# Performance work log

Hardware: AMD Instinct MI355X
Metric: run time of the kernel (lower is better)

The kernel has to match this reference:

```python
import jax, jax.numpy as jnp
import numpy as np

L, H, E, FFN, V, BLOCK = 8, 16, 1024, 4096, 32000, 2048
D = E // H  # head dim = 64
EPS = 1e-5
STD = 0.02

def _ln(x, g, b):
    m = jnp.mean(x, axis=-1, keepdims=True)
    v = jnp.var(x, axis=-1, keepdims=True)
    return (x - m) * jax.lax.rsqrt(v + EPS) * g + b

def setup_inputs() -> dict:
    key = jax.random.key(0)
    ks = jax.random.split(key, 12)
    n = lambda k, shape: (jax.random.normal(k, shape, dtype=jnp.float32) * STD)
    return {
        "idx": jax.random.randint(ks[0], (2, 2048), 0, V),
        "tok_emb": n(ks[1], (V, E)),
        "pos_emb": n(ks[2], (BLOCK, E)),
        # attention weights stored [in, out] so we use x @ W
        "wq": n(ks[3], (L, E, E)),
        "wk": n(ks[4], (L, E, E)),
        "wv": n(ks[5], (L, E, E)),
        "wo": n(ks[6], (L, E, E)),
        "bo": jnp.zeros((L, E), jnp.float32),
        "w1": n(ks[7], (L, E, FFN)),
        "b1": jnp.zeros((L, FFN), jnp.float32),
        "w2": n(ks[8], (L, FFN, E)),
        "b2": jnp.zeros((L, E), jnp.float32),
        "ln1_g": jnp.ones((L, E), jnp.float32),
        "ln1_b": jnp.zeros((L, E), jnp.float32),
        "ln2_g": jnp.ones((L, E), jnp.float32),
        "ln2_b": jnp.zeros((L, E), jnp.float32),
        "lnf_g": jnp.ones((E,), jnp.float32),
        "lnf_b": jnp.zeros((E,), jnp.float32),
    }

def reference(idx, tok_emb, pos_emb, wq, wk, wv, wo, bo, w1, b1, w2, b2,
              ln1_g, ln1_b, ln2_g, ln2_b, lnf_g, lnf_b):
    B, T = idx.shape
    x = tok_emb[idx] + pos_emb[:T]  # [B,T,E]
    causal = jnp.tril(jnp.ones((T, T), dtype=bool))
    scale = 1.0 / np.sqrt(D)

    def step(x, p):
        (wq_, wk_, wv_, wo_, bo_, w1_, b1_, w2_, b2_,
         g1, be1, g2, be2) = p
        h = _ln(x, g1, be1)
        q = (h @ wq_).reshape(B, T, H, D)
        k = (h @ wk_).reshape(B, T, H, D)
        v = (h @ wv_).reshape(B, T, H, D)
        scores = jnp.einsum('bthd,bshd->bhts', q, k) * scale  # [B,H,T,T]
        scores = jnp.where(causal, scores, -jnp.inf)
        w = jax.nn.softmax(scores, axis=-1)
        attn = jnp.einsum('bhts,bshd->bthd', w, v).reshape(B, T, E)
        x = x + attn @ wo_ + bo_
        h2 = _ln(x, g2, be2)
        x = x + jax.nn.relu(h2 @ w1_ + b1_) @ w2_ + b2_
        return x, None

    x, _ = jax.lax.scan(step, x, (wq, wk, wv, wo, bo, w1, b1, w2, b2,
                                  ln1_g, ln1_b, ln2_g, ln2_b))
    x = _ln(x, lnf_g, lnf_b)
    logits = x @ tok_emb.T  # tied weights
    return logits
```

## Files before the change

kernel.cpp:

```cpp
#include <hip/hip_runtime.h>
#include <hip/hip_bf16.h>
#include <cstdint>
#include <cstddef>

#define LAYERS   8
#define HEADS    16
#define EMB      1024
#define FFND     4096
#define VOCAB    32000
#define SEQ      2048
#define NBATCH   2
#define MROWS    (NBATCH*SEQ)
#define HDIM     64
#define QKVSTR   3072
#define LN_EPS   1e-5f

typedef __hip_bfloat16 bf16;
typedef short short8 __attribute__((ext_vector_type(8)));
typedef float f32x4  __attribute__((ext_vector_type(4)));

__device__ __forceinline__ void async_copy16(const bf16* g, bf16* l) {
  __builtin_amdgcn_global_load_lds(
      (const __attribute__((address_space(1))) void*)g,
      (__attribute__((address_space(3))) void*)l, 16, 0, 0);
}

__device__ __forceinline__ uint32_t bfbits(float x) {
  __hip_bfloat16 h = __float2bfloat16(x);
  return (uint32_t)reinterpret_cast<uint16_t&>(h);
}

struct __align__(8) B4 { bf16 a, b, c, d; };

__global__ void k_f32_to_bf16(const float* __restrict__ in, bf16* __restrict__ out, long n4) {
  long i = (long)blockIdx.x * blockDim.x + threadIdx.x;
  const long stride = (long)gridDim.x * blockDim.x;
  for (; i < n4; i += stride) {
    float4 v = reinterpret_cast<const float4*>(in)[i];
    B4 o;
    o.a = __float2bfloat16(v.x);
    o.b = __float2bfloat16(v.y);
    o.c = __float2bfloat16(v.z);
    o.d = __float2bfloat16(v.w);
    reinterpret_cast<B4*>(out)[i] = o;
  }
}

__global__ void k_embed(const int* __restrict__ idx, const float* __restrict__ tok,
                        const float* __restrict__ pos, float* __restrict__ x) {
  const int row  = blockIdx.x;
  const int tpos = row & (SEQ - 1);
  const int token = idx[row];
  const float4* te = (const float4*)(tok + (long)token * EMB);
  const float4* pe = (const float4*)(pos + (long)tpos * EMB);
  float4* xo = (float4*)(x + (long)row * EMB);
  for (int i = threadIdx.x; i < EMB / 4; i += blockDim.x) {
    float4 a = te[i], b = pe[i];
    a.x += b.x; a.y += b.y; a.z += b.z; a.w += b.w;
    xo[i] = a;
  }
}

__global__ void k_transpose_w(const float* __restrict__ in, bf16* __restrict__ out,
                              int K, int N) {
  __shared__ float tile[32][33];
  const int n0 = blockIdx.x * 32, k0 = blockIdx.y * 32;
  const int tx = threadIdx.x, ty = threadIdx.y;
  for (int i = 0; i < 32; i += 8)
    tile[ty + i][tx] = in[(long)(k0 + ty + i) * N + n0 + tx];
  __syncthreads();
  for (int i = 0; i < 32; i += 8)
    out[(long)(n0 + ty + i) * K + k0 + tx] = __float2bfloat16(tile[tx][ty + i]);
}

__global__ void k_transpose_w4(const float* __restrict__ wq, const float* __restrict__ wk,
                               const float* __restrict__ wv, const float* __restrict__ wo,
                               bf16* __restrict__ qkvT, bf16* __restrict__ woT) {
  __shared__ float tile[32][33];
  const float* in;
  bf16* out;
  switch (blockIdx.z) {
    case 0:  in = wq; out = qkvT;               break;
    case 1:  in = wk; out = qkvT + EMB * EMB;   break;
    case 2:  in = wv; out = qkvT + 2 * EMB * EMB; break;
    default: in = wo; out = woT;                break;
  }
  const int n0 = blockIdx.x * 32, k0 = blockIdx.y * 32;
  const int tx = threadIdx.x, ty = threadIdx.y;
  for (int i = 0; i < 32; i += 8)
    tile[ty + i][tx] = in[(long)(k0 + ty + i) * EMB + n0 + tx];
  __syncthreads();
  for (int i = 0; i < 32; i += 8)
    out[(long)(n0 + ty + i) * EMB + k0 + tx] = __float2bfloat16(tile[tx][ty + i]);
}

__global__ void k_transpose_v(const bf16* __restrict__ v, int vstr, bf16* __restrict__ vt) {
  __shared__ bf16 tile[32][33];
  const int bh = blockIdx.z;
  const int b = bh >> 4, h = bh & 15;
  const int t0 = blockIdx.x * 32, d0 = blockIdx.y * 32;
  const int tx = threadIdx.x, ty = threadIdx.y;
  for (int i = 0; i < 32; i += 8)
    tile[ty + i][tx] = v[(long)(b * SEQ + t0 + ty + i) * vstr + h * HDIM + d0 + tx];
  __syncthreads();
  for (int i = 0; i < 32; i += 8)
    vt[(long)(bh * HDIM + d0 + ty + i) * SEQ + t0 + tx] = tile[tx][ty + i];
}

__global__ __launch_bounds__(256)
void k_layernorm(const float* __restrict__ x, const float* __restrict__ g,
                 const float* __restrict__ b, bf16* __restrict__ out) {
  const long row = blockIdx.x;
  const float* xr = x + row * EMB;
  const int t = threadIdx.x;
  float xv[4];
  float s = 0.f, sq = 0.f;
#pragma unroll
  for (int i = 0; i < 4; i++) {
    xv[i] = xr[t + i * 256];
    s += xv[i];
    sq += xv[i] * xv[i];
  }
#pragma unroll
  for (int m = 1; m < 64; m <<= 1) { s += __shfl_xor(s, m); sq += __shfl_xor(sq, m); }
  __shared__ float rs_[4], rq_[4];
  const int wid = t >> 6;
  if ((t & 63) == 0) { rs_[wid] = s; rq_[wid] = sq; }
  __syncthreads();
  s  = rs_[0] + rs_[1] + rs_[2] + rs_[3];
  sq = rq_[0] + rq_[1] + rq_[2] + rq_[3];
  const float mean = s * (1.f / EMB);
  const float var  = sq * (1.f / EMB) - mean * mean;
  const float rstd = rsqrtf(var + LN_EPS);
#pragma unroll
  for (int i = 0; i < 4; i++) {
    const int c = t + i * 256;
    out[row * EMB + c] = __float2bfloat16((xv[i] - mean) * rstd * g[c] + b[c]);
  }
}

template<int MODE>
__global__ __launch_bounds__(512, 2)
void gemm256(const bf16* __restrict__ A, const bf16* __restrict__ Bt,
             int M, int N, int K,
             bf16* __restrict__ outB, float* __restrict__ outF,
             const float* __restrict__ bias) {
  extern __shared__ __align__(16) char smem[];
  char* const smA = smem;
  char* const smB = smem + 65536;

  const int t    = threadIdx.x;
  const int lane = t & 63;
  const int wid  = t >> 6;
  const int wr   = wid >> 2;
  const int wc   = wid & 3;
  const int lrow = lane & 15;
  const int ks16 = (lane >> 4) * 16;
  const int rswz = (lrow & 7) << 4;

  int lin = blockIdx.x * gridDim.y + blockIdx.y;
  { const int nwg = gridDim.x * gridDim.y; const int per = nwg >> 3;
    lin = (lin & 7) * per + (lin >> 3); }
  const int gx8  = gridDim.x * 8;
  const int half = lin / gx8;
  const int rem  = lin - half * gx8;
  const long bm  = (long)(half * 8 + (rem & 7)) * 256;
  const long bn  = (long)(rem >> 3) * 256;
  const int NT = K >> 6;

  const int row0 = wid * 8 + (lane >> 3);
  const int col0 = ((lane & 7) ^ (lane >> 3)) * 8;
  const int row1 = row0 + 64;
  const int dst0 = wid * 1024;
  const int dst1 = 8192 + wid * 1024;
  const bf16* const gA = A  + bm * K;
  const bf16* const gB = Bt + bn * K;

  auto STG = [&](char* ring, const bf16* g_, int tile, int h) {
    char* slot = ring + (((tile << 1) + h) & 3) * 16384;
    const bf16* sb = g_ + ((long)h * 128) * K + (long)tile * 64;
    async_copy16(sb + (long)row0 * K + col0, (bf16*)(slot + dst0));
    async_copy16(sb + (long)row1 * K + col0, (bf16*)(slot + dst1));
  };
  auto LDA8 = [&](int u, int m, int kk) -> short8 {
    const int off = (m * 16 + lrow) * 128 + ((kk * 64 + ks16) ^ rswz);
    return *reinterpret_cast<const short8*>(smA + (((u << 1) + wr) & 3) * 16384 + off);
  };
  auto LDB8 = [&](int u, int n, int kk) -> short8 {
    const int off = ((wc & 1) * 64 + n * 16 + lrow) * 128 + ((kk * 64 + ks16) ^ rswz);
    return *reinterpret_cast<const short8*>(smB + (((u << 1) + (wc >> 1)) & 3) * 16384 + off);
  };
#define MF(a_, b_, c_) __builtin_amdgcn_mfma_f32_16x16x32_bf16(a_, b_, c_, 0, 0, 0)

  f32x4 acc[8][4] = {};

  STG(smB, gB, 0, 0); STG(smB, gB, 0, 1);
  STG(smA, gA, 0, 0); STG(smA, gA, 0, 1);
  STG(smB, gB, 1, 0); STG(smB, gB, 1, 1);
  asm volatile("s_waitcnt vmcnt(4)" ::: "memory");
  __builtin_amdgcn_s_barrier();

  short8 bq[4][2];
  for (int u = 0; u < NT; u++) {
#pragma unroll
    for (int n = 0; n < 4; n++) { bq[n][0] = LDB8(u, n, 0); bq[n][1] = LDB8(u, n, 1); }
    short8 a0 = LDA8(u, 0, 0), a1 = LDA8(u, 0, 1), a2 = LDA8(u, 1, 0), a3 = LDA8(u, 1, 1);
    if (u + 1 < NT) STG(smA, gA, u + 1, 0);
    __builtin_amdgcn_s_barrier();
    asm volatile("s_waitcnt lgkmcnt(0)" ::: "memory");
    __builtin_amdgcn_sched_barrier(0);
    __builtin_amdgcn_s_setprio(1);
#pragma unroll
    for (int n = 0; n < 4; n++) {
      acc[0][n] = MF(a0, bq[n][0], acc[0][n]); acc[0][n] = MF(a1, bq[n][1], acc[0][n]);
      acc[1][n] = MF(a2, bq[n][0], acc[1][n]); acc[1][n] = MF(a3, bq[n][1], acc[1][n]);
    }
    __builtin_amdgcn_s_setprio(0);
    __builtin_amdgcn_s_barrier();

    a0 = LDA8(u, 2, 0); a1 = LDA8(u, 2, 1); a2 = LDA8(u, 3, 0); a3 = LDA8(u, 3, 1);
    if (u + 1 < NT) STG(smA, gA, u + 1, 1);
    __builtin_amdgcn_s_barrier();
    asm volatile("s_waitcnt lgkmcnt(0)" ::: "memory");
    __builtin_amdgcn_sched_barrier(0);
    __builtin_amdgcn_s_setprio(1);
#pragma unroll
    for (int n = 0; n < 4; n++) {
      acc[2][n] = MF(a0, bq[n][0], acc[2][n]); acc[2][n] = MF(a1, bq[n][1], acc[2][n]);
      acc[3][n] = MF(a2, bq[n][0], acc[3][n]); acc[3][n] = MF(a3, bq[n][1], acc[3][n]);
    }
    __builtin_amdgcn_s_setprio(0);
    __builtin_amdgcn_s_barrier();

    a0 = LDA8(u, 4, 0); a1 = LDA8(u, 4, 1); a2 = LDA8(u, 5, 0); a3 = LDA8(u, 5, 1);
    if (u + 2 < NT) STG(smB, gB, u + 2, 0);
    __builtin_amdgcn_s_barrier();
    asm volatile("s_waitcnt lgkmcnt(0)" ::: "memory");
    __builtin_amdgcn_sched_barrier(0);
    __builtin_amdgcn_s_setprio(1);
#pragma unroll
    for (int n = 0; n < 4; n++) {
      acc[4][n] = MF(a0, bq[n][0], acc[4][n]); acc[4][n] = MF(a1, bq[n][1], acc[4][n]);
      acc[5][n] = MF(a2, bq[n][0], acc[5][n]); acc[5][n] = MF(a3, bq[n][1], acc[5][n]);
    }
    __builtin_amdgcn_s_setprio(0);
    __builtin_amdgcn_s_barrier();

    a0 = LDA8(u, 6, 0); a1 = LDA8(u, 6, 1); a2 = LDA8(u, 7, 0); a3 = LDA8(u, 7, 1);
    if (u + 2 < NT) STG(smB, gB, u + 2, 1);
    __builtin_amdgcn_s_barrier();
    asm volatile("s_waitcnt lgkmcnt(0)" ::: "memory");
    __builtin_amdgcn_sched_barrier(0);
    __builtin_amdgcn_s_setprio(1);
#pragma unroll
    for (int n = 0; n < 4; n++) {
      acc[6][n] = MF(a0, bq[n][0], acc[6][n]); acc[6][n] = MF(a1, bq[n][1], acc[6][n]);
      acc[7][n] = MF(a2, bq[n][0], acc[7][n]); acc[7][n] = MF(a3, bq[n][1], acc[7][n]);
    }
    __builtin_amdgcn_s_setprio(0);
    if (u + 2 < NT) { asm volatile("s_waitcnt vmcnt(4)" ::: "memory"); }
    else            { asm volatile("s_waitcnt vmcnt(0)" ::: "memory"); }
    __builtin_amdgcn_s_barrier();
  }

  const long rb = bm + wr * 128 + (lane >> 4) * 4;
  const long cb = bn + wc * 64 + lrow;
#pragma unroll
  for (int m = 0; m < 8; m++) {
#pragma unroll
    for (int n = 0; n < 4; n++) {
      const long col = cb + n * 16;
#pragma unroll
      for (int r = 0; r < 4; r++) {
        const long row = rb + m * 16 + r;
        float v = acc[m][n][r];
        if (MODE == 0) {
          outB[row * N + col] = __float2bfloat16(v);
        } else if (MODE == 2) {
          v += bias[col];
          outB[row * N + col] = __float2bfloat16(v > 0.f ? v : 0.f);
        } else {
          outF[row * N + col] = v;
        }
      }
    }
  }
#undef MF
}

#define BM 128
#define BN 128
#define BK 32

__global__ __launch_bounds__(256)
void gemm_bt(const bf16* __restrict__ A, const bf16* __restrict__ Bt,
             int M, int N, int K,
             float* __restrict__ outF, const float* __restrict__ bias) {
  __shared__ __align__(16) bf16 lA[2][BM * BK];
  __shared__ __align__(16) bf16 lB[2][BN * BK];
  const int t    = threadIdx.x;
  const int lane = t & 63;
  const int wid  = t >> 6;
  const int wr   = wid >> 1;
  const int wc   = wid & 1;
  const long bm  = (long)blockIdx.y * BM;
  const long bn  = (long)blockIdx.x * BN;

  f32x4 acc[4][4] = {};

  const long arow = t >> 2;
  const int  acol = (((t & 3) ^ ((t >> 2) & 3)) * 8);
  const bf16* gA = A  + (bm + arow) * K + acol;
  const bf16* gB = Bt + (bn + arow) * K + acol;
  const long astep = 64L * K;

  auto STGBT = [&](int buf, int k0) {
    async_copy16(gA + k0,         &lA[buf][wid * 512]);
    async_copy16(gA + k0 + astep, &lA[buf][wid * 512 + 2048]);
    async_copy16(gB + k0,         &lB[buf][wid * 512]);
    async_copy16(gB + k0 + astep, &lB[buf][wid * 512 + 2048]);
  };

  STGBT(0, 0);
  __syncthreads();

  int cur = 0;
  for (int k0 = 0; k0 < K; k0 += BK) {
    if (k0 + BK < K) STGBT(cur ^ 1, k0 + BK);

    const int ksel = (((lane >> 4) ^ (lane & 3)) * 8);
    short8 af[4], bfv[4];
#pragma unroll
    for (int i = 0; i < 4; i++) {
      af[i]  = *reinterpret_cast<const short8*>(&lA[cur][(wr * 64 + i * 16 + (lane & 15)) * BK + ksel]);
      bfv[i] = *reinterpret_cast<const short8*>(&lB[cur][(wc * 64 + i * 16 + (lane & 15)) * BK + ksel]);
    }
#pragma unroll
    for (int i = 0; i < 4; i++)
#pragma unroll
      for (int j = 0; j < 4; j++)
        acc[i][j] = __builtin_amdgcn_mfma_f32_16x16x32_bf16(af[i], bfv[j], acc[i][j], 0, 0, 0);
    __syncthreads();
    cur ^= 1;
  }

  const long rbase = bm + wr * 64 + (lane >> 4) * 4;
  const long cbase = bn + wc * 64 + (lane & 15);
#pragma unroll
  for (int i = 0; i < 4; i++) {
#pragma unroll
    for (int j = 0; j < 4; j++) {
      const long col = cbase + j * 16;
#pragma unroll
      for (int r = 0; r < 4; r++) {
        const long row = rbase + i * 16 + r;
        outF[row * N + col] += acc[i][j][r] + bias[col];
      }
    }
  }
}

__global__ __launch_bounds__(256)
void k_attn(const bf16* __restrict__ qkv, const bf16* __restrict__ vt, bf16* __restrict__ o) {
  const int qt = gridDim.x - 1 - blockIdx.x;
  const int bh = blockIdx.y;
  const int b  = bh >> 4;
  const int h  = bh & 15;
  const int t0b = qt * 128;
  const int tid = threadIdx.x;
  const int w    = tid >> 6;
  const int lane = tid & 63;
  const int lg = lane >> 4;
  const int li = lane & 15;
  const int t0w = t0b + w * 32;

  __shared__ __align__(16) bf16 Kl[2][64 * 64];
  __shared__ __align__(16) bf16 Vl[2][64 * 64];
  __shared__ __align__(16) bf16 Pl[4][32 * 64];

  const bf16* qbase = qkv + (long)(b * SEQ) * QKVSTR + h * HDIM;
  const bf16* kbase = qkv + (long)(b * SEQ) * QKVSTR + EMB + h * HDIM;
  const bf16* vbase = vt + (long)bh * HDIM * SEQ;

  short8 qf[2][2];
#pragma unroll
  for (int f = 0; f < 2; f++) {
    const bf16* qrow = qbase + (long)(t0w + f * 16 + li) * QKVSTR;
    qf[f][0] = *reinterpret_cast<const short8*>(&qrow[lg * 8]);
    qf[f][1] = *reinterpret_cast<const short8*>(&qrow[32 + lg * 8]);
  }

  f32x4 oacc[2][4] = {};
  float mrow[2] = {-1e30f, -1e30f}, lrow[2] = {0.f, 0.f};

  const int nkt = (t0b >> 6) + 1;
  const int l8  = lane >> 3;
  const int sl8 = ((lane & 7) ^ l8) * 8;

  char* const Pw = (char*)&Pl[w][0];
  const int pswz = (li & 7) << 4;

#pragma unroll
  for (int sh = 0; sh < 2; sh++) {
    const int r = sh * 32 + w * 8 + l8;
    async_copy16(kbase + (long)r * QKVSTR + sl8, &Kl[0][(sh * 32 + w * 8) * 64]);
    async_copy16(vbase + (long)r * SEQ + sl8,    &Vl[0][(sh * 32 + w * 8) * 64]);
  }
  __syncthreads();

  int cur = 0;
  for (int kt = 0; kt <= nkt; kt++) {
    const int s0 = kt * 64;
    if (kt < nkt) {
      const int s0n = s0 + 64;
      bf16* Kn = &Kl[cur ^ 1][0];
      bf16* Vn = &Vl[cur ^ 1][0];
#pragma unroll
      for (int sh = 0; sh < 2; sh++) {
        const int r = sh * 32 + w * 8 + l8;
        async_copy16(kbase + (long)(s0n + r) * QKVSTR + sl8, Kn + (sh * 32 + w * 8) * 64);
        async_copy16(vbase + (long)r * SEQ + s0n + sl8,      Vn + (sh * 32 + w * 8) * 64);
      }
    }

    f32x4 s[2][4] = {};
#pragma unroll
    for (int kk = 0; kk < 2; kk++)
#pragma unroll
      for (int sf = 0; sf < 4; sf++) {
        const short8 kf = *reinterpret_cast<const short8*>(
            &Kl[cur][(sf * 16 + li) * 64 + ((((kk << 2) | lg) ^ (li & 7)) * 8)]);
        s[0][sf] = __builtin_amdgcn_mfma_f32_16x16x32_bf16(kf, qf[0][kk], s[0][sf], 0, 0, 0);
        s[1][sf] = __builtin_amdgcn_mfma_f32_16x16x32_bf16(kf, qf[1][kk], s[1][sf], 0, 0, 0);
      }

    const bool diag = (kt >= nkt - 1);
#pragma unroll
    for (int f = 0; f < 2; f++)
#pragma unroll
      for (int sf = 0; sf < 4; sf++)
#pragma unroll
        for (int r = 0; r < 4; r++) {
          float val = s[f][sf][r] * 0.18033688011112042f;
          if (diag && (s0 + sf * 16 + lg * 4 + r > t0w + f * 16 + li)) val = -1e30f;
          s[f][sf][r] = val;
        }

#pragma unroll
    for (int f = 0; f < 2; f++) {
      float mx = -1e30f;
#pragma unroll
      for (int sf = 0; sf < 4; sf++)
        mx = fmaxf(mx, fmaxf(fmaxf(s[f][sf][0], s[f][sf][1]), fmaxf(s[f][sf][2], s[f][sf][3])));
      mx = fmaxf(mx, __shfl_xor(mx, 16));
      mx = fmaxf(mx, __shfl_xor(mx, 32));
      const float mnew = fmaxf(mrow[f], mx);
      const float alpha = exp2f(mrow[f] - mnew);
      mrow[f] = mnew;
      float rs = 0.f;
#pragma unroll
      for (int sf = 0; sf < 4; sf++)
#pragma unroll
        for (int r = 0; r < 4; r++) {
          const float pv = exp2f(s[f][sf][r] - mnew);
          s[f][sf][r] = pv;
          rs += pv;
        }
      rs += __shfl_xor(rs, 16);
      rs += __shfl_xor(rs, 32);
      lrow[f] = lrow[f] * alpha + rs;
#pragma unroll
      for (int d = 0; d < 4; d++)
#pragma unroll
        for (int r = 0; r < 4; r++) oacc[f][d][r] *= alpha;

#pragma unroll
      for (int sf = 0; sf < 4; sf++) {
        uint2 pw2;
        pw2.x = (bfbits(s[f][sf][1]) << 16) | bfbits(s[f][sf][0]);
        pw2.y = (bfbits(s[f][sf][3]) << 16) | bfbits(s[f][sf][2]);
        *reinterpret_cast<uint2*>(Pw + (f * 16 + li) * 128 + ((sf * 32 + lg * 8) ^ pswz)) = pw2;
      }
    }

#pragma unroll
    for (int kk = 0; kk < 2; kk++) {
      const short8 pb0 = *reinterpret_cast<const short8*>(
          Pw + li * 128 + ((kk * 64 + lg * 16) ^ pswz));
      const short8 pb1 = *reinterpret_cast<const short8*>(
          Pw + (16 + li) * 128 + ((kk * 64 + lg * 16) ^ pswz));
#pragma unroll
      for (int d = 0; d < 4; d++) {
        const short8 vf = *reinterpret_cast<const short8*>(
            &Vl[cur][(d * 16 + li) * 64 + ((((kk << 2) | lg) ^ (li & 7)) * 8)]);
        oacc[0][d] = __builtin_amdgcn_mfma_f32_16x16x32_bf16(vf, pb0, oacc[0][d], 0, 0, 0);
        oacc[1][d] = __builtin_amdgcn_mfma_f32_16x16x32_bf16(vf, pb1, oacc[1][d], 0, 0, 0);
      }
    }

    __syncthreads();
    cur ^= 1;
  }

#pragma unroll
  for (int f = 0; f < 2; f++) {
    const float inv = 1.f / lrow[f];
    bf16* orow = o + (long)(b * SEQ + t0w + f * 16 + li) * EMB + h * HDIM;
#pragma unroll
    for (int d = 0; d < 4; d++) {
      uint2 ow;
      ow.x = (bfbits(oacc[f][d][1] * inv) << 16) | bfbits(oacc[f][d][0] * inv);
      ow.y = (bfbits(oacc[f][d][3] * inv) << 16) | bfbits(oacc[f][d][2] * inv);
      *reinterpret_cast<uint2*>(&orow[d * 16 + lg * 4]) = ow;
    }
  }
}

extern "C" void kernel_launch(void* const* d_in, const int* in_sizes, int n_in,
                              void* d_out, int out_size, void* d_ws, size_t ws_size,
                              hipStream_t stream) {
  (void)in_sizes; (void)n_in; (void)out_size; (void)ws_size;
  const int*   idx = (const int*)  d_in[0];
  const float* tok = (const float*)d_in[1];
  const float* pos = (const float*)d_in[2];
  const float* wq  = (const float*)d_in[3];
  const float* wk  = (const float*)d_in[4];
  const float* wv  = (const float*)d_in[5];
  const float* wo  = (const float*)d_in[6];
  const float* bo  = (const float*)d_in[7];
  const float* w1  = (const float*)d_in[8];
  const float* b1  = (const float*)d_in[9];
  const float* w2  = (const float*)d_in[10];
  const float* b2  = (const float*)d_in[11];
  const float* g1  = (const float*)d_in[12];
  const float* be1 = (const float*)d_in[13];
  const float* g2  = (const float*)d_in[14];
  const float* be2 = (const float*)d_in[15];
  const float* gf  = (const float*)d_in[16];
  const float* bef = (const float*)d_in[17];
  float* out = (float*)d_out;

  (void)hipFuncSetAttribute((const void*)gemm256<0>, hipFuncAttributeMaxDynamicSharedMemorySize, 131072);
  (void)hipFuncSetAttribute((const void*)gemm256<2>, hipFuncAttributeMaxDynamicSharedMemorySize, 131072);
  (void)hipFuncSetAttribute((const void*)gemm256<3>, hipFuncAttributeMaxDynamicSharedMemorySize, 131072);

  char* p = (char*)d_ws;
  auto take = [&p](size_t bytes) { char* r = p; p += (bytes + 255) & ~(size_t)255; return r; };
  float* xf   = (float*)take((size_t)MROWS * EMB * 4);
  bf16*  hb   = (bf16*) take((size_t)MROWS * EMB * 2);
  bf16*  qkvb = (bf16*) take((size_t)MROWS * QKVSTR * 2);
  bf16*  vtb  = (bf16*) take((size_t)MROWS * EMB * 2);
  bf16*  ab   = (bf16*) take((size_t)MROWS * EMB * 2);
  bf16*  fb   = (bf16*) take((size_t)MROWS * FFND * 2);
  bf16*  wqkvT= (bf16*) take((size_t)QKVSTR * EMB * 2);
  bf16*  woT  = (bf16*) take((size_t)EMB * EMB * 2);
  bf16*  w1T  = (bf16*) take((size_t)FFND * EMB * 2);
  bf16*  w2T  = (bf16*) take((size_t)EMB * FFND * 2);
  bf16*  tokT = (bf16*) take((size_t)VOCAB * EMB * 2);

  k_f32_to_bf16<<<2048, 256, 0, stream>>>(tok, tokT, (long)VOCAB * EMB / 4);
  k_embed<<<MROWS, 256, 0, stream>>>(idx, tok, pos, xf);

  const dim3 tb(32, 8);

  for (int l = 0; l < LAYERS; l++) {
    const size_t we = (size_t)l * EMB * EMB;
    const size_t wfo = (size_t)l * EMB * FFND;
    k_transpose_w4<<<dim3(EMB / 32, EMB / 32, 4), tb, 0, stream>>>(
        wq + we, wk + we, wv + we, wo + we, wqkvT, woT);
    k_transpose_w<<<dim3(FFND / 32, EMB / 32),  tb, 0, stream>>>(w1 + wfo, w1T, EMB,  FFND);
    k_transpose_w<<<dim3(EMB / 32,  FFND / 32), tb, 0, stream>>>(w2 + wfo, w2T, FFND, EMB);

    k_layernorm<<<MROWS, 256, 0, stream>>>(xf, g1 + l * EMB, be1 + l * EMB, hb);
    gemm256<0><<<dim3(QKVSTR / 256, MROWS / 256), 512, 131072, stream>>>(
        hb, wqkvT, MROWS, QKVSTR, EMB, qkvb, nullptr, nullptr);
    k_transpose_v<<<dim3(SEQ / 32, HDIM / 32, NBATCH * HEADS), tb, 0, stream>>>(qkvb + 2 * EMB, QKVSTR, vtb);
    k_attn<<<dim3(SEQ / 128, NBATCH * HEADS), 256, 0, stream>>>(qkvb, vtb, ab);
    gemm_bt<<<dim3(EMB / BN, MROWS / BM), 256, 0, stream>>>(ab, woT, MROWS, EMB, EMB, xf, bo + l * EMB);
    k_layernorm<<<MROWS, 256, 0, stream>>>(xf, g2 + l * EMB, be2 + l * EMB, hb);
    gemm256<2><<<dim3(FFND / 256, MROWS / 256), 512, 131072, stream>>>(
        hb, w1T, MROWS, FFND, EMB, fb, nullptr, b1 + l * FFND);
    gemm_bt<<<dim3(EMB / BN, MROWS / BM), 256, 0, stream>>>(fb, w2T, MROWS, EMB, FFND, xf, b2 + l * EMB);
  }

  k_layernorm<<<MROWS, 256, 0, stream>>>(xf, gf, bef, hb);
  gemm256<3><<<dim3(VOCAB / 256, MROWS / 256), 512, 131072, stream>>>(
      hb, tokT, MROWS, VOCAB, EMB, nullptr, out, nullptr);
}
```

Baseline: 3.020 ms.

## Split-K residual GEMMs with atomics, fold Q scale, lazy softmax rescaling

The Wo and W2 residual GEMMs are split over K into two z-slices that accumulate into the fp32 residual with atomic adds. This doubles the grid from 256 blocks so more compute units stay busy. The softmax scale is folded into the Q projection epilogue, so attention only masks diagonal tiles. The online-softmax rescale now runs only when some row max grows by more than 8, which skips most alpha multiplies at the cost of atomic traffic and bounded numeric drift.

New measurement: 2.713 ms. -10.2%, faster.

```diff
diff --git a/kernel.cpp b/kernel.cpp
--- a/kernel.cpp
+++ b/kernel.cpp
@@ -14,6 +14,7 @@
 #define HDIM     64
 #define QKVSTR   3072
 #define LN_EPS   1e-5f
+#define QSCALE   0.18033688011112042f
 
 typedef __hip_bfloat16 bf16;
 typedef short short8 __attribute__((ext_vector_type(8)));
@@ -275,6 +276,7 @@
         const long row = rb + m * 16 + r;
         float v = acc[m][n][r];
         if (MODE == 0) {
+          if (col < EMB) v *= QSCALE;
           outB[row * N + col] = __float2bfloat16(v);
         } else if (MODE == 2) {
           v += bias[col];
@@ -305,13 +307,15 @@
   const int wc   = wid & 1;
   const long bm  = (long)blockIdx.y * BM;
   const long bn  = (long)blockIdx.x * BN;
+  const int  kz  = blockIdx.z;
+  const int  Kh  = K >> 1;
 
   f32x4 acc[4][4] = {};
 
   const long arow = t >> 2;
   const int  acol = (((t & 3) ^ ((t >> 2) & 3)) * 8);
-  const bf16* gA = A  + (bm + arow) * K + acol;
-  const bf16* gB = Bt + (bn + arow) * K + acol;
+  const bf16* gA = A  + (bm + arow) * K + kz * Kh + acol;
+  const bf16* gB = Bt + (bn + arow) * K + kz * Kh + acol;
   const long astep = 64L * K;
 
   auto STGBT = [&](int buf, int k0) {
@@ -325,8 +329,8 @@
   __syncthreads();
 
   int cur = 0;
-  for (int k0 = 0; k0 < K; k0 += BK) {
-    if (k0 + BK < K) STGBT(cur ^ 1, k0 + BK);
+  for (int k0 = 0; k0 < Kh; k0 += BK) {
+    if (k0 + BK < Kh) STGBT(cur ^ 1, k0 + BK);
 
     const int ksel = (((lane >> 4) ^ (lane & 3)) * 8);
     short8 af[4], bfv[4];
@@ -351,10 +355,11 @@
 #pragma unroll
     for (int j = 0; j < 4; j++) {
       const long col = cbase + j * 16;
+      const float bv = kz ? 0.f : bias[col];
 #pragma unroll
       for (int r = 0; r < 4; r++) {
         const long row = rbase + i * 16 + r;
-        outF[row * N + col] += acc[i][j][r] + bias[col];
+        unsafeAtomicAdd(&outF[row * N + col], acc[i][j][r] + bv);
       }
     }
   }
@@ -435,16 +440,15 @@
       }
 
     const bool diag = (kt >= nkt - 1);
-#pragma unroll
-    for (int f = 0; f < 2; f++)
-#pragma unroll
-      for (int sf = 0; sf < 4; sf++)
-#pragma unroll
-        for (int r = 0; r < 4; r++) {
-          float val = s[f][sf][r] * 0.18033688011112042f;
-          if (diag && (s0 + sf * 16 + lg * 4 + r > t0w + f * 16 + li)) val = -1e30f;
-          s[f][sf][r] = val;
-        }
+    if (diag) {
+#pragma unroll
+      for (int f = 0; f < 2; f++)
+#pragma unroll
+        for (int sf = 0; sf < 4; sf++)
+#pragma unroll
+          for (int r = 0; r < 4; r++)
+            if (s0 + sf * 16 + lg * 4 + r > t0w + f * 16 + li) s[f][sf][r] = -1e30f;
+    }
 
 #pragma unroll
     for (int f = 0; f < 2; f++) {
@@ -454,25 +458,28 @@
         mx = fmaxf(mx, fmaxf(fmaxf(s[f][sf][0], s[f][sf][1]), fmaxf(s[f][sf][2], s[f][sf][3])));
       mx = fmaxf(mx, __shfl_xor(mx, 16));
       mx = fmaxf(mx, __shfl_xor(mx, 32));
-      const float mnew = fmaxf(mrow[f], mx);
-      const float alpha = exp2f(mrow[f] - mnew);
-      mrow[f] = mnew;
+      if (__any(mx > mrow[f] + 8.f)) {
+        const float mnew = fmaxf(mrow[f], mx);
+        const float alpha = exp2f(mrow[f] - mnew);
+        mrow[f] = mnew;
+        lrow[f] *= alpha;
+#pragma unroll
+        for (int d = 0; d < 4; d++)
+#pragma unroll
+          for (int r = 0; r < 4; r++) oacc[f][d][r] *= alpha;
+      }
       float rs = 0.f;
 #pragma unroll
       for (int sf = 0; sf < 4; sf++)
 #pragma unroll
         for (int r = 0; r < 4; r++) {
-          const float pv = exp2f(s[f][sf][r] - mnew);
+          const float pv = exp2f(s[f][sf][r] - mrow[f]);
           s[f][sf][r] = pv;
           rs += pv;
         }
       rs += __shfl_xor(rs, 16);
       rs += __shfl_xor(rs, 32);
-      lrow[f] = lrow[f] * alpha + rs;
-#pragma unroll
-      for (int d = 0; d < 4; d++)
-#pragma unroll
-        for (int r = 0; r < 4; r++) oacc[f][d][r] *= alpha;
+      lrow[f] += rs;
 
 #pragma unroll
       for (int sf = 0; sf < 4; sf++) {
@@ -576,11 +583,11 @@
         hb, wqkvT, MROWS, QKVSTR, EMB, qkvb, nullptr, nullptr);
     k_transpose_v<<<dim3(SEQ / 32, HDIM / 32, NBATCH * HEADS), tb, 0, stream>>>(qkvb + 2 * EMB, QKVSTR, vtb);
     k_attn<<<dim3(SEQ / 128, NBATCH * HEADS), 256, 0, stream>>>(qkvb, vtb, ab);
-    gemm_bt<<<dim3(EMB / BN, MROWS / BM), 256, 0, stream>>>(ab, woT, MROWS, EMB, EMB, xf, bo + l * EMB);
+    gemm_bt<<<dim3(EMB / BN, MROWS / BM, 2), 256, 0, stream>>>(ab, woT, MROWS, EMB, EMB, xf, bo + l * EMB);
     k_layernorm<<<MROWS, 256, 0, stream>>>(xf, g2 + l * EMB, be2 + l * EMB, hb);
     gemm256<2><<<dim3(FFND / 256, MROWS / 256), 512, 131072, stream>>>(
         hb, w1T, MROWS, FFND, EMB, fb, nullptr, b1 + l * FFND);
-    gemm_bt<<<dim3(EMB / BN, MROWS / BM), 256, 0, stream>>>(fb, w2T, MROWS, EMB, FFND, xf, b2 + l * EMB);
+    gemm_bt<<<dim3(EMB / BN, MROWS / BM, 2), 256, 0, stream>>>(fb, w2T, MROWS, EMB, FFND, xf, b2 + l * EMB);
   }
 
   k_layernorm<<<MROWS, 256, 0, stream>>>(xf, gf, bef, hb);
```
